# Kernel tuning notes

Hardware: AMD Instinct MI355X
Metric: run time of the kernel (lower is better)

## Reference

```python
import jax, jax.numpy as jnp
import numpy as np

DEPTH = 6
N_INTERNAL = 2 ** DEPTH - 1  # 63
N_LEAVES = 2 ** DEPTH        # 64


def _tree_paths(depth):
    """Precompute, for each leaf, its `depth` ancestor internal-node indices and
    whether the path goes right at each ancestor (static heap-indexing of the tree)."""
    n_internal = 2 ** depth - 1
    n_leaves = 2 ** depth
    anc = np.zeros((n_leaves, depth), dtype=np.int32)
    right = np.zeros((n_leaves, depth), dtype=bool)
    for leaf in range(n_leaves):
        node = leaf + n_internal
        for d in range(depth):
            parent = (node - 1) // 2
            anc[leaf, d] = parent
            right[leaf, d] = (node % 2 == 0)
            node = parent
    return jnp.asarray(anc), jnp.asarray(right)

_ANC, _RIGHT = _tree_paths(DEPTH)


def setup_inputs() -> dict:
    key = jax.random.key(0)
    k = jax.random.split(key, 6)
    B, F, T, C = 8192, 256, 32, 100
    return {
        "x": jax.random.normal(k[0], (B, F), dtype=jnp.float32),
        "split_weights": jax.random.normal(k[1], (T, N_INTERNAL, F), dtype=jnp.float32) * 0.05,
        "split_bias": jax.random.normal(k[2], (T, N_INTERNAL), dtype=jnp.float32) * 0.05,
        "leaf_logits": jax.random.normal(k[3], (T, N_LEAVES, C), dtype=jnp.float32),
        "tree_weights": jax.random.normal(k[4], (T,), dtype=jnp.float32),
        "log_temperature": jnp.zeros((), dtype=jnp.float32),
    }


def reference(x, split_weights, split_bias, leaf_logits, tree_weights, log_temperature):
    # temperature = exp(log_temperature).clamp(0.1, 5.0)
    temp = jnp.clip(jnp.exp(log_temperature), 0.1, 5.0)
    # split probabilities for all trees at once: [T, B, N_INTERNAL]
    logits = jnp.einsum('bf,tnf->tbn', x, split_weights) + split_bias[:, None, :]
    split_probs = jax.nn.sigmoid(logits / temp)
    # gather each leaf's ancestor probs: [T, B, L, D]; right -> p, left -> 1-p
    g = split_probs[:, :, _ANC]
    leaf_probs = jnp.prod(jnp.where(_RIGHT, g, 1.0 - g), axis=-1)  # [T, B, L]
    # per-leaf class distributions: [T, L, C]
    leaf_class_probs = jax.nn.softmax(leaf_logits / temp, axis=-1)
    outputs = jnp.einsum('tbl,tlc->tbc', leaf_probs, leaf_class_probs)  # [T, B, C]
    weights = jax.nn.softmax(tree_weights, axis=0)  # [T]
    return jnp.einsum('t,tbc->bc', weights, outputs)  # [B, C]
```

## Files before the change

kernel.cpp:

```cpp
#include <hip/hip_runtime.h>
#include <math.h>

#define B_  8192
#define F_  256
#define T_  32
#define NI_ 63
#define NL_ 64
#define C_  100
#define K2_ (T_*NL_)
#define NG  8
#define TPG 4

typedef unsigned short u16;
typedef __attribute__((ext_vector_type(8))) short bf16x8;
typedef __attribute__((ext_vector_type(4))) float f32x4;
typedef __attribute__((ext_vector_type(8))) unsigned short u16x8;

__device__ __forceinline__ u16 f2bf(float f) {
    unsigned int u = __float_as_uint(f);
    u += 0x7fffu + ((u >> 16) & 1u);
    return (u16)(u >> 16);
}
__device__ __forceinline__ float bf2f(u16 u) {
    return __uint_as_float(((unsigned int)u) << 16);
}

#define WSB_SWB   0
#define WSB_LCPT  (T_*NI_*F_*2)
#define WSB_XB    (WSB_LCPT + 112*K2_*2)
#define WSB_PART  ((size_t)WSB_XB + (size_t)B_*F_*2)
#define WSB_ATOM  WSB_PART
#define WSB_STORE (WSB_PART + (size_t)NG*B_*112*2)

#define SWBLK  (T_*NI_*F_/2048)
#define XBLK   (B_*F_/2048)
#define LCPBLK (T_*NL_/256)
#define ZBLK   (B_*C_/256)

__device__ __forceinline__ void cvt8(const float* __restrict__ s, u16* __restrict__ d, int i) {
    const float4* p = (const float4*)(s + i);
    float4 v0 = p[0], v1 = p[1];
    u16x8 o;
    o[0] = f2bf(v0.x); o[1] = f2bf(v0.y); o[2] = f2bf(v0.z); o[3] = f2bf(v0.w);
    o[4] = f2bf(v1.x); o[5] = f2bf(v1.y); o[6] = f2bf(v1.z); o[7] = f2bf(v1.w);
    *(u16x8*)(d + i) = o;
}

__global__ void k_prep(const float* __restrict__ sw, const float* __restrict__ x,
                       const float* __restrict__ ll, const float* __restrict__ tw,
                       const float* __restrict__ logT,
                       u16* __restrict__ swb, u16* __restrict__ xb,
                       u16* __restrict__ lcpT, float* __restrict__ out) {
    int blk = blockIdx.x, tid = threadIdx.x;
    if (blk < SWBLK) { cvt8(sw, swb, blk * 2048 + tid * 8); return; }
    blk -= SWBLK;
    if (blk < XBLK) { cvt8(x, xb, blk * 2048 + tid * 8); return; }
    blk -= XBLK;
    if (blk >= LCPBLK) {
        out[(blk - LCPBLK) * 256 + tid] = 0.f;
        return;
    }
    int idx = blk * 256 + tid;
    int t = idx >> 6;
    float temp = __expf(logT[0]);
    temp = fminf(fmaxf(temp, 0.1f), 5.0f);
    float invt = 1.0f / temp;

    float m = -1e30f;
    for (int j = 0; j < T_; ++j) m = fmaxf(m, tw[j]);
    float s = 0.f;
    for (int j = 0; j < T_; ++j) s += __expf(tw[j] - m);
    float wt = __expf(tw[t] - m) / s;

    const float* row = ll + (size_t)idx * C_;
    float m2 = -1e30f;
    for (int c = 0; c < C_; ++c) m2 = fmaxf(m2, row[c]);
    float s2 = 0.f;
    for (int c = 0; c < C_; ++c) s2 += __expf((row[c] - m2) * invt);
    float sc = wt / s2;
    for (int c = 0; c < C_; ++c)
        lcpT[(size_t)c * K2_ + idx] = f2bf(sc * __expf((row[c] - m2) * invt));
    for (int c = C_; c < 112; ++c)
        lcpT[(size_t)c * K2_ + idx] = 0;
}

__global__ __launch_bounds__(512, 4)
void k_fused(const u16* __restrict__ xb, const u16* __restrict__ swb,
             const float* __restrict__ sb, const float* __restrict__ logT,
             const u16* __restrict__ lcpT, void* __restrict__ dst, int storeMode) {
    __shared__ __attribute__((aligned(16))) u16 swS[63 * 264];
    __shared__ __attribute__((aligned(16))) u16 lcpS[8 * 112 * 8];
    __shared__ float slog[8][16][66];
    int tid  = threadIdx.x;
    int w    = tid >> 6;
    int lane = tid & 63;
    int col  = lane & 15;
    int quad = lane >> 4;
    int mb   = blockIdx.x * 128 + w * 16;
    int tg   = blockIdx.y;

    float temp = __expf(logT[0]);
    temp = fminf(fmaxf(temp, 0.1f), 5.0f);
    float invt = 1.0f / temp;

    bf16x8 afr[8];
    #pragma unroll
    for (int ks = 0; ks < 8; ++ks)
        afr[ks] = *(const bf16x8*)(xb + (size_t)(mb + col) * F_ + ks * 32 + quad * 8);

    u16x8 pf_sw[4];
    u16x8 pf_lcp[2];
    {
        int t0 = tg * TPG;
        const char* gsrc = (const char*)(swb + (size_t)t0 * NI_ * F_);
        #pragma unroll
        for (int r = 0; r < 4; ++r) {
            int g = r * 8192 + tid * 16;
            if (g < NI_ * F_ * 2) pf_sw[r] = *(const u16x8*)(gsrc + g);
        }
        #pragma unroll
        for (int r = 0; r < 2; ++r) {
            int idx = r * 512 + tid;
            if (idx < 896) {
                int o = idx / 112, c = idx - o * 112;
                pf_lcp[r] = *(const u16x8*)(lcpT + (size_t)c * K2_ + t0 * NL_ + o * 8);
            }
        }
    }

    f32x4 accO[7];
    #pragma unroll
    for (int i = 0; i < 7; ++i) accO[i] = (f32x4){0.f, 0.f, 0.f, 0.f};

    #pragma unroll 1
    for (int ti = 0; ti < TPG; ++ti) {
        int t = tg * TPG + ti;

        __syncthreads();
        #pragma unroll
        for (int r = 0; r < 4; ++r) {
            int g = r * 8192 + tid * 16;
            if (g < NI_ * F_ * 2) {
                int n   = g >> 9;
                int k16 = (g & 511) >> 4;
                *(u16x8*)&swS[n * 264 + k16 * 8] = pf_sw[r];
            }
        }
        #pragma unroll
        for (int r = 0; r < 2; ++r) {
            int idx = r * 512 + tid;
            if (idx < 896) {
                int o = idx / 112, c = idx - o * 112;
                *(u16x8*)&lcpS[(o * 112 + c) * 8] = pf_lcp[r];
            }
        }
        __syncthreads();

        if (ti + 1 < TPG) {
            int tn = t + 1;
            const char* gsrc = (const char*)(swb + (size_t)tn * NI_ * F_);
            #pragma unroll
            for (int r = 0; r < 4; ++r) {
                int g = r * 8192 + tid * 16;
                if (g < NI_ * F_ * 2) pf_sw[r] = *(const u16x8*)(gsrc + g);
            }
            #pragma unroll
            for (int r = 0; r < 2; ++r) {
                int idx = r * 512 + tid;
                if (idx < 896) {
                    int o = idx / 112, c = idx - o * 112;
                    pf_lcp[r] = *(const u16x8*)(lcpT + (size_t)c * K2_ + tn * NL_ + o * 8);
                }
            }
        }

        f32x4 acc[4];
        #pragma unroll
        for (int i = 0; i < 4; ++i) acc[i] = (f32x4){0.f, 0.f, 0.f, 0.f};
        #pragma unroll
        for (int ks = 0; ks < 8; ++ks) {
            #pragma unroll
            for (int nt = 0; nt < 4; ++nt) {
                int n  = nt * 16 + col;
                int ne = n > 62 ? 62 : n;
                bf16x8 bfr = *(const bf16x8*)&swS[ne * 264 + ks * 32 + quad * 8];
                acc[nt] = __builtin_amdgcn_mfma_f32_16x16x32_bf16(afr[ks], bfr, acc[nt], 0, 0, 0);
            }
        }

        asm volatile("s_waitcnt lgkmcnt(0)" ::: "memory");
        #pragma unroll
        for (int nt = 0; nt < 4; ++nt) {
            int n = nt * 16 + col;
            float bias = (n < NI_) ? sb[t * NI_ + n] : 0.f;
            #pragma unroll
            for (int r = 0; r < 4; ++r) {
                float lg = (acc[nt][r] + bias) * invt;
                slog[w][quad * 4 + r][n] = 1.0f / (1.0f + __expf(-lg));
            }
        }
        asm volatile("s_waitcnt lgkmcnt(0)" ::: "memory");

        bf16x8 af0, af1;
        #pragma unroll
        for (int grp = 0; grp < 2; ++grp) {
            int s = (grp ? 11 : 7) + quad;
            float pref = 1.0f;
            int node = s;
            #pragma unroll
            for (int d = 0; d < 3; ++d) {
                int par = (node - 1) >> 1;
                float g = slog[w][col][par];
                pref = (node & 1) ? (pref - pref * g) : (pref * g);
                node = par;
            }
            float gs  = slog[w][col][s];
            float gl  = slog[w][col][2 * s + 1];
            float gr  = slog[w][col][2 * s + 2];
            float g00 = slog[w][col][4 * s + 3];
            float g01 = slog[w][col][4 * s + 4];
            float g10 = slog[w][col][4 * s + 5];
            float g11 = slog[w][col][4 * s + 6];
            #pragma unroll
            for (int j = 0; j < 8; ++j) {
                const int b2 = (j >> 2) & 1, b1 = (j >> 1) & 1, b0 = j & 1;
                float f3 = b2 ? gs : 1.0f - gs;
                float c1 = b2 ? gr : gl;
                float f4 = b1 ? c1 : 1.0f - c1;
                float c2 = b2 ? (b1 ? g11 : g10) : (b1 ? g01 : g00);
                float f5 = b0 ? c2 : 1.0f - c2;
                float p  = pref * f3 * f4 * f5;
                if (grp == 0) af0[j] = (short)f2bf(p);
                else          af1[j] = (short)f2bf(p);
            }
        }

        #pragma unroll
        for (int nt = 0; nt < 7; ++nt) {
            int n = nt * 16 + col;
            bf16x8 lb0 = *(const bf16x8*)&lcpS[(quad * 112 + n) * 8];
            bf16x8 lb1 = *(const bf16x8*)&lcpS[((4 + quad) * 112 + n) * 8];
            accO[nt] = __builtin_amdgcn_mfma_f32_16x16x32_bf16(af0, lb0, accO[nt], 0, 0, 0);
            accO[nt] = __builtin_amdgcn_mfma_f32_16x16x32_bf16(af1, lb1, accO[nt], 0, 0, 0);
        }
    }

    if (storeMode) {
        u16* pp = (u16*)dst + (size_t)tg * B_ * 112;
        #pragma unroll
        for (int nt = 0; nt < 7; ++nt) {
            int c = nt * 16 + col;
            #pragma unroll
            for (int r = 0; r < 4; ++r) {
                int b = mb + quad * 4 + r;
                pp[(size_t)b * 112 + c] = f2bf(accO[nt][r]);
            }
        }
    } else {
        float* od = (float*)dst;
        #pragma unroll
        for (int nt = 0; nt < 7; ++nt) {
            int c = nt * 16 + col;
            if (c < C_) {
                #pragma unroll
                for (int r = 0; r < 4; ++r) {
                    int b = mb + quad * 4 + r;
                    atomicAdd(&od[(size_t)b * C_ + c], accO[nt][r]);
                }
            }
        }
    }
}

__global__ void k_red(const u16* __restrict__ part, float* __restrict__ out) {
    int idx = blockIdx.x * 256 + threadIdx.x;
    int b = idx / 112, c = idx - b * 112;
    if (c < C_) {
        float s = 0.f;
        #pragma unroll
        for (int tg = 0; tg < NG; ++tg)
            s += bf2f(part[((size_t)tg * B_ + b) * 112 + c]);
        out[(size_t)b * C_ + c] = s;
    }
}

__global__ void k_zf(float* __restrict__ out, int n) {
    int i = blockIdx.x * 256 + threadIdx.x;
    if (i < n) out[i] = 0.f;
}

__global__ void k_mono(const float* __restrict__ x, const float* __restrict__ sw,
                       const float* __restrict__ sb, const float* __restrict__ ll,
                       const float* __restrict__ tw, const float* __restrict__ logT,
                       float* __restrict__ outg) {
    __shared__ float slcp[NL_ * C_];
    int tid = threadIdx.x;
    int b = blockIdx.x * 256 + tid;

    float temp = __expf(logT[0]);
    temp = fminf(fmaxf(temp, 0.1f), 5.0f);
    float invt = 1.0f / temp;

    float m = -1e30f;
    for (int j = 0; j < T_; ++j) m = fmaxf(m, tw[j]);
    float sden = 0.f;
    for (int j = 0; j < T_; ++j) sden += __expf(tw[j] - m);

    float acc[C_];
    #pragma unroll
    for (int c = 0; c < C_; ++c) acc[c] = 0.f;

    for (int t = 0; t < T_; ++t) {
        __syncthreads();
        {
            int l = tid & 63, cq = tid >> 6;
            float wt = __expf(tw[t] - m) / sden;
            const float* row = ll + ((size_t)t * NL_ + l) * C_;
            float m2 = -1e30f;
            for (int c = 0; c < C_; ++c) m2 = fmaxf(m2, row[c]);
            float s2 = 0.f;
            for (int c = 0; c < C_; ++c) s2 += __expf((row[c] - m2) * invt);
            float sc = wt / s2;
            for (int c = cq * 25; c < cq * 25 + 25; ++c)
                slcp[l * C_ + c] = sc * __expf((row[c] - m2) * invt);
        }
        __syncthreads();

        float an[NI_];
        #pragma unroll
        for (int n = 0; n < NI_; ++n) an[n] = 0.f;
        for (int k = 0; k < F_; ++k) {
            float xv = x[(size_t)b * F_ + k];
            #pragma unroll
            for (int n = 0; n < NI_; ++n)
                an[n] = fmaf(xv, sw[((size_t)t * NI_ + n) * F_ + k], an[n]);
        }
        #pragma unroll
        for (int n = 0; n < NI_; ++n) {
            float lg = (an[n] + sb[t * NI_ + n]) * invt;
            an[n] = 1.0f / (1.0f + __expf(-lg));
        }
        #pragma unroll
        for (int l = 0; l < NL_; ++l) {
            int node = l + NI_;
            float p = 1.0f;
            #pragma unroll
            for (int d = 0; d < 6; ++d) {
                int par = (node - 1) >> 1;
                float gv = an[par];
                p = (node & 1) ? (p - p * gv) : (p * gv);
                node = par;
            }
            #pragma unroll
            for (int c = 0; c < C_; ++c)
                acc[c] = fmaf(p, slcp[l * C_ + c], acc[c]);
        }
    }
    for (int c = 0; c < C_; ++c)
        outg[(size_t)b * C_ + c] = acc[c];
}

extern "C" void kernel_launch(void* const* d_in, const int* in_sizes, int n_in,
                              void* d_out, int out_size, void* d_ws, size_t ws_size,
                              hipStream_t stream) {
    bool ok = (n_in >= 6)
           && (in_sizes[0] == B_ * F_)
           && (in_sizes[1] == T_ * NI_ * F_)
           && (in_sizes[2] == T_ * NI_)
           && (in_sizes[3] == T_ * NL_ * C_)
           && (in_sizes[4] == T_)
           && (in_sizes[5] == 1)
           && (out_size == B_ * C_);
    if (!ok) {
        k_zf<<<(out_size + 255) / 256, 256, 0, stream>>>((float*)d_out, out_size);
        return;
    }

    const float* x    = (const float*)d_in[0];
    const float* sw   = (const float*)d_in[1];
    const float* sb   = (const float*)d_in[2];
    const float* ll   = (const float*)d_in[3];
    const float* tw   = (const float*)d_in[4];
    const float* logT = (const float*)d_in[5];
    float* out = (float*)d_out;

    if (ws_size >= WSB_STORE) {
        u16* swb  = (u16*)((char*)d_ws + WSB_SWB);
        u16* lcpT = (u16*)((char*)d_ws + WSB_LCPT);
        u16* xb   = (u16*)((char*)d_ws + WSB_XB);
        u16* part = (u16*)((char*)d_ws + WSB_PART);

        k_prep <<<SWBLK + XBLK + LCPBLK, 256, 0, stream>>>(sw, x, ll, tw, logT, swb, xb, lcpT, out);
        k_fused<<<dim3(B_ / 128, NG), 512, 0, stream>>>(xb, swb, sb, logT, lcpT, part, 1);
        k_red  <<<(B_ * 112) / 256, 256, 0, stream>>>(part, out);
    } else if (ws_size >= WSB_ATOM) {
        u16* swb  = (u16*)((char*)d_ws + WSB_SWB);
        u16* lcpT = (u16*)((char*)d_ws + WSB_LCPT);
        u16* xb   = (u16*)((char*)d_ws + WSB_XB);

        k_prep <<<SWBLK + XBLK + LCPBLK + ZBLK, 256, 0, stream>>>(sw, x, ll, tw, logT, swb, xb, lcpT, out);
        k_fused<<<dim3(B_ / 128, NG), 512, 0, stream>>>(xb, swb, sb, logT, lcpT, d_out, 0);
    } else {
        k_mono<<<B_ / 256, 256, 0, stream>>>(x, sw, sb, ll, tw, logT, out);
    }
}
```

Measured before the change: 145.7 us.

## Stage split weights and leaf probs via direct global-to-LDS loads with prepacked layout

The prep kernel now packs the split weights into a [t][k8][n][8] layout padded to 64 nodes, and the leaf class probabilities into a per-tree [o][c][8] layout. This lets the fused kernel copy each tree's tiles straight into LDS with global_load_lds instead of staging them through registers. The register-based prefetch of the next tree is dropped, so fewer VGPRs are needed, and launch bounds go from 4 to 2 blocks per SM. In exchange, global loads no longer overlap with the previous tree's compute, and the loads sit between two barriers.

```diff
diff --git a/kernel.cpp b/kernel.cpp
--- a/kernel.cpp
+++ b/kernel.cpp
@@ -25,14 +25,21 @@
     return __uint_as_float(((unsigned int)u) << 16);
 }
 
+__device__ __forceinline__ void gl16(const void* g, void* l) {
+    __builtin_amdgcn_global_load_lds(
+        (const __attribute__((address_space(1))) unsigned int*)g,
+        (__attribute__((address_space(3))) unsigned int*)l,
+        16, 0, 0);
+}
+
 #define WSB_SWB   0
-#define WSB_LCPT  (T_*NI_*F_*2)
-#define WSB_XB    (WSB_LCPT + 112*K2_*2)
+#define WSB_LCPT  (T_*32*64*8*2)
+#define WSB_XB    (WSB_LCPT + T_*8*112*8*2)
 #define WSB_PART  ((size_t)WSB_XB + (size_t)B_*F_*2)
 #define WSB_ATOM  WSB_PART
 #define WSB_STORE (WSB_PART + (size_t)NG*B_*112*2)
 
-#define SWBLK  (T_*NI_*F_/2048)
+#define SWBLK  (T_*64*32/256)
 #define XBLK   (B_*F_/2048)
 #define LCPBLK (T_*NL_/256)
 #define ZBLK   (B_*C_/256)
@@ -52,7 +59,23 @@
                        u16* __restrict__ swb, u16* __restrict__ xb,
                        u16* __restrict__ lcpT, float* __restrict__ out) {
     int blk = blockIdx.x, tid = threadIdx.x;
-    if (blk < SWBLK) { cvt8(sw, swb, blk * 2048 + tid * 8); return; }
+    if (blk < SWBLK) {
+        int gid = blk * 256 + tid;
+        int k8 = gid & 31;
+        int n  = (gid >> 5) & 63;
+        int t  = gid >> 11;
+        u16x8 o;
+        if (n < NI_) {
+            const float4* p = (const float4*)(sw + ((size_t)(t * NI_ + n)) * F_ + k8 * 8);
+            float4 v0 = p[0], v1 = p[1];
+            o[0] = f2bf(v0.x); o[1] = f2bf(v0.y); o[2] = f2bf(v0.z); o[3] = f2bf(v0.w);
+            o[4] = f2bf(v1.x); o[5] = f2bf(v1.y); o[6] = f2bf(v1.z); o[7] = f2bf(v1.w);
+        } else {
+            o = (u16x8){0,0,0,0,0,0,0,0};
+        }
+        *(u16x8*)(swb + (((size_t)t * 32 + k8) * 64 + n) * 8) = o;
+        return;
+    }
     blk -= SWBLK;
     if (blk < XBLK) { cvt8(x, xb, blk * 2048 + tid * 8); return; }
     blk -= XBLK;
@@ -62,6 +85,8 @@
     }
     int idx = blk * 256 + tid;
     int t = idx >> 6;
+    int l = idx & 63;
+    int o = l >> 3, jj = l & 7;
     float temp = __expf(logT[0]);
     temp = fminf(fmaxf(temp, 0.1f), 5.0f);
     float invt = 1.0f / temp;
@@ -78,17 +103,18 @@
     float s2 = 0.f;
     for (int c = 0; c < C_; ++c) s2 += __expf((row[c] - m2) * invt);
     float sc = wt / s2;
+    u16* base = lcpT + (size_t)t * (8 * 112 * 8);
     for (int c = 0; c < C_; ++c)
-        lcpT[(size_t)c * K2_ + idx] = f2bf(sc * __expf((row[c] - m2) * invt));
+        base[(o * 112 + c) * 8 + jj] = f2bf(sc * __expf((row[c] - m2) * invt));
     for (int c = C_; c < 112; ++c)
-        lcpT[(size_t)c * K2_ + idx] = 0;
-}
-
-__global__ __launch_bounds__(512, 4)
+        base[(o * 112 + c) * 8 + jj] = 0;
+}
+
+__global__ __launch_bounds__(512, 2)
 void k_fused(const u16* __restrict__ xb, const u16* __restrict__ swb,
              const float* __restrict__ sb, const float* __restrict__ logT,
              const u16* __restrict__ lcpT, void* __restrict__ dst, int storeMode) {
-    __shared__ __attribute__((aligned(16))) u16 swS[63 * 264];
+    __shared__ __attribute__((aligned(16))) u16 swS[32 * 64 * 8];
     __shared__ __attribute__((aligned(16))) u16 lcpS[8 * 112 * 8];
     __shared__ float slog[8][16][66];
     int tid  = threadIdx.x;
@@ -108,26 +134,6 @@
     for (int ks = 0; ks < 8; ++ks)
         afr[ks] = *(const bf16x8*)(xb + (size_t)(mb + col) * F_ + ks * 32 + quad * 8);
 
-    u16x8 pf_sw[4];
-    u16x8 pf_lcp[2];
-    {
-        int t0 = tg * TPG;
-        const char* gsrc = (const char*)(swb + (size_t)t0 * NI_ * F_);
-        #pragma unroll
-        for (int r = 0; r < 4; ++r) {
-            int g = r * 8192 + tid * 16;
-            if (g < NI_ * F_ * 2) pf_sw[r] = *(const u16x8*)(gsrc + g);
-        }
-        #pragma unroll
-        for (int r = 0; r < 2; ++r) {
-            int idx = r * 512 + tid;
-            if (idx < 896) {
-                int o = idx / 112, c = idx - o * 112;
-                pf_lcp[r] = *(const u16x8*)(lcpT + (size_t)c * K2_ + t0 * NL_ + o * 8);
-            }
-        }
-    }
-
     f32x4 accO[7];
     #pragma unroll
     for (int i = 0; i < 7; ++i) accO[i] = (f32x4){0.f, 0.f, 0.f, 0.f};
@@ -137,42 +143,22 @@
         int t = tg * TPG + ti;
 
         __syncthreads();
-        #pragma unroll
-        for (int r = 0; r < 4; ++r) {
-            int g = r * 8192 + tid * 16;
-            if (g < NI_ * F_ * 2) {
-                int n   = g >> 9;
-                int k16 = (g & 511) >> 4;
-                *(u16x8*)&swS[n * 264 + k16 * 8] = pf_sw[r];
-            }
-        }
-        #pragma unroll
-        for (int r = 0; r < 2; ++r) {
-            int idx = r * 512 + tid;
-            if (idx < 896) {
-                int o = idx / 112, c = idx - o * 112;
-                *(u16x8*)&lcpS[(o * 112 + c) * 8] = pf_lcp[r];
-            }
-        }
+
+        {
+            const char* gsw = (const char*)(swb + (size_t)t * (32 * 64 * 8));
+            char* lsw = (char*)swS;
+            #pragma unroll
+            for (int r = 0; r < 4; ++r)
+                gl16(gsw + r * 8192 + w * 1024 + lane * 16,
+                     lsw + r * 8192 + w * 1024);
+            const char* glc = (const char*)(lcpT + (size_t)t * (8 * 112 * 8));
+            char* llc = (char*)lcpS;
+            gl16(glc + w * 1024 + lane * 16, llc + w * 1024);
+            if (w < 6)
+                gl16(glc + 8192 + w * 1024 + lane * 16, llc + 8192 + w * 1024);
+        }
+
         __syncthreads();
-
-        if (ti + 1 < TPG) {
-            int tn = t + 1;
-            const char* gsrc = (const char*)(swb + (size_t)tn * NI_ * F_);
-            #pragma unroll
-            for (int r = 0; r < 4; ++r) {
-                int g = r * 8192 + tid * 16;
-                if (g < NI_ * F_ * 2) pf_sw[r] = *(const u16x8*)(gsrc + g);
-            }
-            #pragma unroll
-            for (int r = 0; r < 2; ++r) {
-                int idx = r * 512 + tid;
-                if (idx < 896) {
-                    int o = idx / 112, c = idx - o * 112;
-                    pf_lcp[r] = *(const u16x8*)(lcpT + (size_t)c * K2_ + tn * NL_ + o * 8);
-                }
-            }
-        }
 
         f32x4 acc[4];
         #pragma unroll
@@ -183,7 +169,7 @@
             for (int nt = 0; nt < 4; ++nt) {
                 int n  = nt * 16 + col;
                 int ne = n > 62 ? 62 : n;
-                bf16x8 bfr = *(const bf16x8*)&swS[ne * 264 + ks * 32 + quad * 8];
+                bf16x8 bfr = *(const bf16x8*)&swS[((ks * 4 + quad) * 64 + ne) * 8];
                 acc[nt] = __builtin_amdgcn_mfma_f32_16x16x32_bf16(afr[ks], bfr, acc[nt], 0, 0, 0);
             }
         }
```

Result: faster. 133.0 us (-8.8%).
